# Kernel optimization log

Measured on AMD Instinct MI355X. Metric: run time of the kernel, lower is better.

Reference implementation:

```python
import jax, jax.numpy as jnp
import numpy as np


def setup_inputs() -> dict:
    key = jax.random.key(0)
    ks = jax.random.split(key, 9)
    B, H = 8192, 1024
    scale = 1.0 / np.sqrt(4 * H)
    return {
        "h": jax.random.normal(ks[0], (B, H), jnp.float32),
        "x": jax.random.normal(ks[1], (B, 2 * H), jnp.float32),
        "glo": jax.random.normal(ks[2], (B, H), jnp.float32),
        "Wi_w": jax.random.normal(ks[3], (H, 4 * H), jnp.float32) * scale,
        "Wi_b": jnp.zeros((H,), jnp.float32),
        "Wf_w": jax.random.normal(ks[4], (H, 4 * H), jnp.float32) * scale,
        "Wf_b": jnp.zeros((H,), jnp.float32),
        "Wc_w": jax.random.normal(ks[5], (H, 4 * H), jnp.float32) * scale,
        "Wc_b": jnp.zeros((H,), jnp.float32),
    }


def reference(h, x, glo, Wi_w, Wi_b, Wf_w, Wf_b, Wc_w, Wc_b):
    # Dropout is identity in eval mode (deterministic reference).
    cat_all = jnp.concatenate([h, x, glo], axis=-1)  # [B, 4H]
    # Fused gate GEMM: stack the three weight matrices, one matmul.
    W = jnp.concatenate([Wi_w, Wf_w, Wc_w], axis=0)      # [3H, 4H]
    b = jnp.concatenate([Wi_b, Wf_b, Wc_b], axis=0)      # [3H]
    gates = cat_all @ W.T + b                             # [B, 3H]
    H = h.shape[-1]
    i = jax.nn.sigmoid(gates[:, :H])
    f = jax.nn.sigmoid(gates[:, H:2 * H])
    c = jnp.tanh(gates[:, 2 * H:])
    # 2-way softmax over (i, f): alpha0 = exp(i)/(exp(i)+exp(f)) = sigmoid(i-f)
    alpha0 = jax.nn.sigmoid(i - f)
    output = alpha0 * c + (1.0 - alpha0) * h
    return output
```

## Files before the change

### kernel.cpp

```cpp
#include <hip/hip_runtime.h>

typedef unsigned short USHORT;
typedef short bf16x8 __attribute__((ext_vector_type(8)));
typedef float f32x4 __attribute__((ext_vector_type(4)));

__device__ __forceinline__ USHORT f2bf(float f) {
    unsigned u = __float_as_uint(f);
    u += 0x7fffu + ((u >> 16) & 1u);
    return (USHORT)(u >> 16);
}
__device__ __forceinline__ float bf2f(USHORT s) {
    return __uint_as_float(((unsigned)s) << 16);
}
__device__ __forceinline__ float sigm(float v) { return 1.f / (1.f + __expf(-v)); }
__device__ __forceinline__ float mytanh(float v) { return 1.f - 2.f / (__expf(2.f * v) + 1.f); }

using gcu32p = const unsigned int __attribute__((address_space(1))) *;
using lu32p  = unsigned int __attribute__((address_space(3))) *;

__device__ __forceinline__ void load_lds16(const void* g, void* l) {
    __builtin_amdgcn_global_load_lds((gcu32p)g, (lu32p)l, 16, 0, 0);
}

__global__ __launch_bounds__(256) void conv_all(const float* __restrict__ h,
                                                const float* __restrict__ x,
                                                const float* __restrict__ glo,
                                                const float* __restrict__ Wi,
                                                const float* __restrict__ Wf,
                                                const float* __restrict__ Wc,
                                                USHORT* __restrict__ A,
                                                USHORT* __restrict__ W) {
    int bid = blockIdx.x;
    if (bid < 16384) {
        int idx = (bid * 256 + threadIdx.x) * 8;
        int m = idx >> 12, k = idx & 4095;
        const float* s;
        if (k < 1024)      s = h   + (size_t)m * 1024 + k;
        else if (k < 3072) s = x   + (size_t)m * 2048 + (k - 1024);
        else               s = glo + (size_t)m * 1024 + (k - 3072);
        float4 f0 = ((const float4*)s)[0];
        float4 f1 = ((const float4*)s)[1];
        union { USHORT us[8]; uint4 v; } u;
        u.us[0] = f2bf(f0.x); u.us[1] = f2bf(f0.y); u.us[2] = f2bf(f0.z); u.us[3] = f2bf(f0.w);
        u.us[4] = f2bf(f1.x); u.us[5] = f2bf(f1.y); u.us[6] = f2bf(f1.z); u.us[7] = f2bf(f1.w);
        *(uint4*)(A + idx) = u.v;
    } else {
        int idx = ((bid - 16384) * 256 + threadIdx.x) * 8;
        int n = idx >> 12, k = idx & 4095;
        const float* base = (n < 1024) ? Wi : (n < 2048 ? Wf : Wc);
        const float* s = base + (size_t)(n & 1023) * 4096 + k;
        float4 f0 = ((const float4*)s)[0];
        float4 f1 = ((const float4*)s)[1];
        union { USHORT us[8]; uint4 v; } u;
        u.us[0] = f2bf(f0.x); u.us[1] = f2bf(f0.y); u.us[2] = f2bf(f0.z); u.us[3] = f2bf(f0.w);
        u.us[4] = f2bf(f1.x); u.us[5] = f2bf(f1.y); u.us[6] = f2bf(f1.z); u.us[7] = f2bf(f1.w);
        *(uint4*)(W + idx) = u.v;
    }
}


#define A_ELEMS 16384
#define B_ELEMS 12288

template<int ISS, int WMODE>
__device__ __forceinline__ void do_tile(const USHORT* aRd, const USHORT* bRd,
                                        USHORT* aWr, USHORT* bWr,
                                        const USHORT* (&aG)[4], const USHORT* (&bG)[3],
                                        int koff0, f32x4 (&acc)[8][3]) {
    bf16x8 bv[3][2];
    #pragma unroll
    for (int q = 0; q < 4; ++q) {
        bf16x8 av[2][2];
        #pragma unroll
        for (int m2 = 0; m2 < 2; ++m2)
            #pragma unroll
            for (int kh = 0; kh < 2; ++kh)
                av[m2][kh] = *(const bf16x8*)(aRd + (q * 32 + m2 * 16) * 64 + (koff0 ^ (kh * 32)));
        if (q == 0) {
            #pragma unroll
            for (int nt = 0; nt < 3; ++nt)
                #pragma unroll
                for (int kh = 0; kh < 2; ++kh)
                    bv[nt][kh] = *(const bf16x8*)(bRd + nt * 16 * 64 + (koff0 ^ (kh * 32)));
        }
        if (ISS) {
            if (q == 0) {
                load_lds16(aG[0], aWr);
                load_lds16(aG[1], aWr + 4096);
                aG[0] += 64; aG[1] += 64;
            } else if (q == 1) {
                load_lds16(aG[2], aWr + 8192);
                load_lds16(aG[3], aWr + 12288);
                aG[2] += 64; aG[3] += 64;
            } else if (q == 2) {
                load_lds16(bG[0], bWr);
                load_lds16(bG[1], bWr + 4096);
                bG[0] += 64; bG[1] += 64;
            } else {
                load_lds16(bG[2], bWr + 8192);
                bG[2] += 64;
            }
        }
        __builtin_amdgcn_sched_barrier(0);
        __builtin_amdgcn_s_barrier();
        __builtin_amdgcn_s_setprio(1);
        #pragma unroll
        for (int m2 = 0; m2 < 2; ++m2)
            #pragma unroll
            for (int nt = 0; nt < 3; ++nt)
                #pragma unroll
                for (int kh = 0; kh < 2; ++kh)
                    acc[q * 2 + m2][nt] = __builtin_amdgcn_mfma_f32_16x16x32_bf16(
                        av[m2][kh], bv[nt][kh], acc[q * 2 + m2][nt], 0, 0, 0);
        __builtin_amdgcn_s_setprio(0);
        if (q == 3) {
            if (WMODE == 0) asm volatile("s_waitcnt vmcnt(7)" ::: "memory");
            else if (WMODE == 1) asm volatile("s_waitcnt vmcnt(0)" ::: "memory");
        }
        __builtin_amdgcn_s_barrier();
    }
}

__global__ __launch_bounds__(512, 2) void gemm8p(const USHORT* __restrict__ A,
                                                 const USHORT* __restrict__ B,
                                                 const float* __restrict__ bi,
                                                 const float* __restrict__ bfp,
                                                 const float* __restrict__ bc,
                                                 USHORT* __restrict__ gates) {
    __shared__ __align__(16) USHORT As[3 * 256 * 64];
    __shared__ __align__(16) USHORT Bs[2 * 192 * 64];

    const int tid  = threadIdx.x;
    const int lane = tid & 63, wv = tid >> 6;
    const int s  = (blockIdx.x & 7) * 64 + (blockIdx.x >> 3);
    const int m0 = (s & 31) * 256;
    const int n0 = (s >> 5) * 192;

    const int wM = wv >> 2, wN = wv & 3;
    const int lm = lane & 15;
    const int gw = lane >> 4;
    const int koff0 = ((gw ^ (lm >> 1)) & 7) * 8;
    const int wvOff = wv * 512;
    const int aOff = (wM * 128 + lm) * 64;
    const int bOff = (wN * 48 + lm) * 64;

    const int gswz = ((lane & 7) ^ (4 * (wv & 1) + (lane >> 4))) & 7;
    const USHORT* aG[4];
    const USHORT* bG[3];
    #pragma unroll
    for (int j = 0; j < 4; ++j)
        aG[j] = A + (size_t)(m0 + j * 64 + wv * 8 + (lane >> 3)) * 4096 + gswz * 8;
    #pragma unroll
    for (int t = 0; t < 3; ++t)
        bG[t] = B + (size_t)(n0 + t * 64 + wv * 8 + (lane >> 3)) * 4096 + gswz * 8;

    f32x4 acc[8][3];
    #pragma unroll
    for (int a = 0; a < 8; ++a)
        #pragma unroll
        for (int b = 0; b < 3; ++b) {
            f32x4 z = {0.f, 0.f, 0.f, 0.f};
            acc[a][b] = z;
        }

    USHORT* aB0 = As;
    USHORT* aB1 = As + A_ELEMS;
    USHORT* aB2 = As + 2 * A_ELEMS;
    USHORT* bB0 = Bs;
    USHORT* bB1 = Bs + B_ELEMS;

    #pragma unroll
    for (int j = 0; j < 4; ++j) { load_lds16(aG[j], aB0 + j * 4096 + wvOff); aG[j] += 64; }
    #pragma unroll
    for (int t = 0; t < 3; ++t) { load_lds16(bG[t], bB0 + t * 4096 + wvOff); bG[t] += 64; }
    #pragma unroll
    for (int j = 0; j < 4; ++j) { load_lds16(aG[j], aB1 + j * 4096 + wvOff); aG[j] += 64; }
    #pragma unroll
    for (int t = 0; t < 3; ++t) { load_lds16(bG[t], bB1 + t * 4096 + wvOff); bG[t] += 64; }
    asm volatile("s_waitcnt vmcnt(7)" ::: "memory");
    __builtin_amdgcn_s_barrier();

    for (int kt = 0; kt < 62; ++kt) {
        do_tile<1, 0>(aB0 + aOff, bB0 + bOff, aB2 + wvOff, bB0 + wvOff,
                      aG, bG, koff0, acc);
        USHORT* tp = aB0; aB0 = aB1; aB1 = aB2; aB2 = tp;
        tp = bB0; bB0 = bB1; bB1 = tp;
    }
    do_tile<0, 1>(aB0 + aOff, bB0 + bOff, As, Bs, aG, bG, koff0, acc);
    do_tile<0, 2>(aB1 + aOff, bB1 + bOff, As, Bs, aG, bG, koff0, acc);

    #pragma unroll
    for (int nt = 0; nt < 3; ++nt) {
        int gc = n0 + wN * 48 + nt * 16 + lm;
        float bb = (gc < 1024) ? bi[gc] : (gc < 2048 ? bfp[gc - 1024] : bc[gc - 2048]);
        #pragma unroll
        for (int mt = 0; mt < 8; ++mt) {
            #pragma unroll
            for (int r = 0; r < 4; ++r) {
                int lrow = wM * 128 + mt * 16 + (lane >> 4) * 4 + r;
                gates[(size_t)(m0 + lrow) * 3072 + gc] = f2bf(acc[mt][nt][r] + bb);
            }
        }
    }
}

__global__ __launch_bounds__(256) void epi(const USHORT* __restrict__ gates,
                                           const float* __restrict__ h,
                                           float* __restrict__ out) {
    int e = (blockIdx.x * 256 + threadIdx.x) * 8;
    int m = e >> 10, n = e & 1023;
    const USHORT* gp = gates + (size_t)m * 3072 + n;
    union { USHORT us[8]; uint4 v; } gi, gf, gc;
    gi.v = *(const uint4*)(gp);
    gf.v = *(const uint4*)(gp + 1024);
    gc.v = *(const uint4*)(gp + 2048);
    const float* hp = h + (size_t)m * 1024 + n;
    float4 h0 = ((const float4*)hp)[0];
    float4 h1 = ((const float4*)hp)[1];
    float hv[8] = {h0.x, h0.y, h0.z, h0.w, h1.x, h1.y, h1.z, h1.w};
    float o[8];
    #pragma unroll
    for (int j = 0; j < 8; ++j) {
        float iv = sigm(bf2f(gi.us[j]));
        float fv = sigm(bf2f(gf.us[j]));
        float cv = mytanh(bf2f(gc.us[j]));
        float al = sigm(iv - fv);
        o[j] = al * cv + (1.f - al) * hv[j];
    }
    float4* op = (float4*)(out + (size_t)m * 1024 + n);
    op[0] = make_float4(o[0], o[1], o[2], o[3]);
    op[1] = make_float4(o[4], o[5], o[6], o[7]);
}

__global__ __launch_bounds__(256) void gemm3_noconv(const float* __restrict__ h,
                                                    const float* __restrict__ x,
                                                    const float* __restrict__ glo,
                                                    const float* __restrict__ Wi,
                                                    const float* __restrict__ Wf,
                                                    const float* __restrict__ Wc,
                                                    const float* __restrict__ bi,
                                                    const float* __restrict__ bfp,
                                                    const float* __restrict__ bc,
                                                    float* __restrict__ out) {
    __shared__ USHORT At[128 * 32];
    __shared__ USHORT Bt[128 * 32];
    __shared__ USHORT stash[128 * 136];

    const int tid  = threadIdx.x;
    const int lane = tid & 63, wv = tid >> 6;
    const int n0 = blockIdx.x * 128;
    const int m0 = blockIdx.y * 128;
    const int wM = wv >> 1, wN = wv & 1;
    const int lm = lane & 15, qk = (lane >> 4) * 8;
    const int rowS = tid >> 1;
    const int colS = (tid & 1) * 16;

    for (int p = 0; p < 3; ++p) {
        f32x4 acc[4][4];
        #pragma unroll
        for (int a = 0; a < 4; ++a)
            #pragma unroll
            for (int b = 0; b < 4; ++b) {
                f32x4 z = {0.f, 0.f, 0.f, 0.f};
                acc[a][b] = z;
            }
        const float* Wg = (p == 0) ? Wi : (p == 1 ? Wf : Wc);

        for (int kt = 0; kt < 128; ++kt) {
            __syncthreads();
            int k = kt * 32 + colS;
            const float* s;
            if (k < 1024)      s = h   + (size_t)(m0 + rowS) * 1024 + k;
            else if (k < 3072) s = x   + (size_t)(m0 + rowS) * 2048 + (k - 1024);
            else               s = glo + (size_t)(m0 + rowS) * 1024 + (k - 3072);
            float4 f0 = ((const float4*)s)[0], f1 = ((const float4*)s)[1];
            float4 f2 = ((const float4*)s)[2], f3 = ((const float4*)s)[3];
            union { USHORT us[8]; uint4 v; } u0, u1;
            u0.us[0]=f2bf(f0.x); u0.us[1]=f2bf(f0.y); u0.us[2]=f2bf(f0.z); u0.us[3]=f2bf(f0.w);
            u0.us[4]=f2bf(f1.x); u0.us[5]=f2bf(f1.y); u0.us[6]=f2bf(f1.z); u0.us[7]=f2bf(f1.w);
            u1.us[0]=f2bf(f2.x); u1.us[1]=f2bf(f2.y); u1.us[2]=f2bf(f2.z); u1.us[3]=f2bf(f2.w);
            u1.us[4]=f2bf(f3.x); u1.us[5]=f2bf(f3.y); u1.us[6]=f2bf(f3.z); u1.us[7]=f2bf(f3.w);
            *(uint4*)(At + rowS * 32 + colS)     = u0.v;
            *(uint4*)(At + rowS * 32 + colS + 8) = u1.v;
            const float* sw = Wg + (size_t)(n0 + rowS) * 4096 + k;
            float4 w0 = ((const float4*)sw)[0], w1 = ((const float4*)sw)[1];
            float4 w2 = ((const float4*)sw)[2], w3 = ((const float4*)sw)[3];
            union { USHORT us[8]; uint4 v; } v0, v1;
            v0.us[0]=f2bf(w0.x); v0.us[1]=f2bf(w0.y); v0.us[2]=f2bf(w0.z); v0.us[3]=f2bf(w0.w);
            v0.us[4]=f2bf(w1.x); v0.us[5]=f2bf(w1.y); v0.us[6]=f2bf(w1.z); v0.us[7]=f2bf(w1.w);
            v1.us[0]=f2bf(w2.x); v1.us[1]=f2bf(w2.y); v1.us[2]=f2bf(w2.z); v1.us[3]=f2bf(w2.w);
            v1.us[4]=f2bf(w3.x); v1.us[5]=f2bf(w3.y); v1.us[6]=f2bf(w3.z); v1.us[7]=f2bf(w3.w);
            *(uint4*)(Bt + rowS * 32 + colS)     = v0.v;
            *(uint4*)(Bt + rowS * 32 + colS + 8) = v1.v;
            __syncthreads();

            bf16x8 av[4], bv[4];
            #pragma unroll
            for (int mt = 0; mt < 4; ++mt)
                av[mt] = *(const bf16x8*)(At + (wM * 64 + mt * 16 + lm) * 32 + qk);
            #pragma unroll
            for (int nt = 0; nt < 4; ++nt)
                bv[nt] = *(const bf16x8*)(Bt + (wN * 64 + nt * 16 + lm) * 32 + qk);
            #pragma unroll
            for (int mt = 0; mt < 4; ++mt)
                #pragma unroll
                for (int nt = 0; nt < 4; ++nt)
                    acc[mt][nt] = __builtin_amdgcn_mfma_f32_16x16x32_bf16(
                        av[mt], bv[nt], acc[mt][nt], 0, 0, 0);
        }

        const float* bias = (p == 0) ? bi : (p == 1 ? bfp : bc);
        #pragma unroll
        for (int nt = 0; nt < 4; ++nt) {
            int lcol = wN * 64 + nt * 16 + lm;
            float bb = bias[n0 + lcol];
            #pragma unroll
            for (int mt = 0; mt < 4; ++mt) {
                #pragma unroll
                for (int r = 0; r < 4; ++r) {
                    int lrow = wM * 64 + mt * 16 + (lane >> 4) * 4 + r;
                    float g = acc[mt][nt][r] + bb;
                    int li = lrow * 136 + lcol;
                    if (p == 0) {
                        stash[li] = f2bf(sigm(g));
                    } else if (p == 1) {
                        float iv = bf2f(stash[li]);
                        stash[li] = f2bf(sigm(iv - sigm(g)));
                    } else {
                        float al = bf2f(stash[li]);
                        float cv = mytanh(g);
                        size_t gi = (size_t)(m0 + lrow) * 1024 + (n0 + lcol);
                        out[gi] = al * cv + (1.f - al) * h[gi];
                    }
                }
            }
        }
    }
}

extern "C" void kernel_launch(void* const* d_in, const int* in_sizes, int n_in,
                              void* d_out, int out_size, void* d_ws, size_t ws_size,
                              hipStream_t stream) {
    const float* h   = (const float*)d_in[0];
    const float* x   = (const float*)d_in[1];
    const float* glo = (const float*)d_in[2];
    const float* Wi  = (const float*)d_in[3];
    const float* bi  = (const float*)d_in[4];
    const float* Wf  = (const float*)d_in[5];
    const float* bfp = (const float*)d_in[6];
    const float* Wc  = (const float*)d_in[7];
    const float* bc  = (const float*)d_in[8];
    float* out = (float*)d_out;

    const size_t szA = (size_t)8192 * 4096 * 2;
    const size_t szW = (size_t)3072 * 4096 * 2;
    const size_t szG = (size_t)8192 * 3072 * 2;

    if (ws_size >= szA + szW + szG) {
        USHORT* Abf = (USHORT*)d_ws;
        USHORT* Wbf = (USHORT*)((char*)d_ws + szA);
        USHORT* Gbf = (USHORT*)((char*)d_ws + szA + szW);
        conv_all<<<16384 + 6144, 256, 0, stream>>>(h, x, glo, Wi, Wf, Wc, Abf, Wbf);
        gemm8p<<<512, 512, 0, stream>>>(Abf, Wbf, bi, bfp, bc, Gbf);
        epi<<<4096, 256, 0, stream>>>(Gbf, h, out);
    } else {
        gemm3_noconv<<<dim3(8, 64), 256, 0, stream>>>(
            h, x, glo, Wi, Wf, Wc, bi, bfp, bc, out);
    }
}
```

Baseline: 448.2 us.

## Fuse gate epilogue into GEMM by interleaving i/f/c weight tiles per block

Each GEMM block's 192-column N tile is remapped into three 64-column slices taken from the i, f and c gate weights at the same hidden index. Each thread therefore holds all three gate pre-activations and can apply sigmoid, tanh and the blend with h directly. This removes the bf16 gates buffer in the workspace, its write and reread, and the separate epilogue launch. In exchange, the epilogue's h loads and fp32 output stores are strided per lane rather than vectorized.

Result: faster. 423.6 us (-5.5%).

```diff
diff --git a/kernel.cpp b/kernel.cpp
--- a/kernel.cpp
+++ b/kernel.cpp
@@ -81,7 +81,7 @@
             for (int nt = 0; nt < 3; ++nt)
                 #pragma unroll
                 for (int kh = 0; kh < 2; ++kh)
-                    bv[nt][kh] = *(const bf16x8*)(bRd + nt * 16 * 64 + (koff0 ^ (kh * 32)));
+                    bv[nt][kh] = *(const bf16x8*)(bRd + nt * 4096 + (koff0 ^ (kh * 32)));
         }
         if (ISS) {
             if (q == 0) {
@@ -121,12 +121,13 @@
     }
 }
 
-__global__ __launch_bounds__(512, 2) void gemm8p(const USHORT* __restrict__ A,
-                                                 const USHORT* __restrict__ B,
-                                                 const float* __restrict__ bi,
-                                                 const float* __restrict__ bfp,
-                                                 const float* __restrict__ bc,
-                                                 USHORT* __restrict__ gates) {
+__global__ __launch_bounds__(512, 2) void gemm_fused(const USHORT* __restrict__ A,
+                                                     const USHORT* __restrict__ B,
+                                                     const float* __restrict__ bi,
+                                                     const float* __restrict__ bfp,
+                                                     const float* __restrict__ bc,
+                                                     const float* __restrict__ h,
+                                                     float* __restrict__ out) {
     __shared__ __align__(16) USHORT As[3 * 256 * 64];
     __shared__ __align__(16) USHORT Bs[2 * 192 * 64];
 
@@ -134,7 +135,7 @@
     const int lane = tid & 63, wv = tid >> 6;
     const int s  = (blockIdx.x & 7) * 64 + (blockIdx.x >> 3);
     const int m0 = (s & 31) * 256;
-    const int n0 = (s >> 5) * 192;
+    const int n0 = (s >> 5) * 64;
 
     const int wM = wv >> 2, wN = wv & 3;
     const int lm = lane & 15;
@@ -142,7 +143,7 @@
     const int koff0 = ((gw ^ (lm >> 1)) & 7) * 8;
     const int wvOff = wv * 512;
     const int aOff = (wM * 128 + lm) * 64;
-    const int bOff = (wN * 48 + lm) * 64;
+    const int bOff = (wN * 16 + lm) * 64;
 
     const int gswz = ((lane & 7) ^ (4 * (wv & 1) + (lane >> 4))) & 7;
     const USHORT* aG[4];
@@ -152,7 +153,7 @@
         aG[j] = A + (size_t)(m0 + j * 64 + wv * 8 + (lane >> 3)) * 4096 + gswz * 8;
     #pragma unroll
     for (int t = 0; t < 3; ++t)
-        bG[t] = B + (size_t)(n0 + t * 64 + wv * 8 + (lane >> 3)) * 4096 + gswz * 8;
+        bG[t] = B + (size_t)(t * 1024 + n0 + wv * 8 + (lane >> 3)) * 4096 + gswz * 8;
 
     f32x4 acc[8][3];
     #pragma unroll
@@ -189,47 +190,24 @@
     do_tile<0, 1>(aB0 + aOff, bB0 + bOff, As, Bs, aG, bG, koff0, acc);
     do_tile<0, 2>(aB1 + aOff, bB1 + bOff, As, Bs, aG, bG, koff0, acc);
 
-    #pragma unroll
-    for (int nt = 0; nt < 3; ++nt) {
-        int gc = n0 + wN * 48 + nt * 16 + lm;
-        float bb = (gc < 1024) ? bi[gc] : (gc < 2048 ? bfp[gc - 1024] : bc[gc - 2048]);
-        #pragma unroll
-        for (int mt = 0; mt < 8; ++mt) {
-            #pragma unroll
-            for (int r = 0; r < 4; ++r) {
-                int lrow = wM * 128 + mt * 16 + (lane >> 4) * 4 + r;
-                gates[(size_t)(m0 + lrow) * 3072 + gc] = f2bf(acc[mt][nt][r] + bb);
-            }
-        }
-    }
-}
-
-__global__ __launch_bounds__(256) void epi(const USHORT* __restrict__ gates,
-                                           const float* __restrict__ h,
-                                           float* __restrict__ out) {
-    int e = (blockIdx.x * 256 + threadIdx.x) * 8;
-    int m = e >> 10, n = e & 1023;
-    const USHORT* gp = gates + (size_t)m * 3072 + n;
-    union { USHORT us[8]; uint4 v; } gi, gf, gc;
-    gi.v = *(const uint4*)(gp);
-    gf.v = *(const uint4*)(gp + 1024);
-    gc.v = *(const uint4*)(gp + 2048);
-    const float* hp = h + (size_t)m * 1024 + n;
-    float4 h0 = ((const float4*)hp)[0];
-    float4 h1 = ((const float4*)hp)[1];
-    float hv[8] = {h0.x, h0.y, h0.z, h0.w, h1.x, h1.y, h1.z, h1.w};
-    float o[8];
-    #pragma unroll
-    for (int j = 0; j < 8; ++j) {
-        float iv = sigm(bf2f(gi.us[j]));
-        float fv = sigm(bf2f(gf.us[j]));
-        float cv = mytanh(bf2f(gc.us[j]));
-        float al = sigm(iv - fv);
-        o[j] = al * cv + (1.f - al) * hv[j];
-    }
-    float4* op = (float4*)(out + (size_t)m * 1024 + n);
-    op[0] = make_float4(o[0], o[1], o[2], o[3]);
-    op[1] = make_float4(o[4], o[5], o[6], o[7]);
+    const int nc = n0 + wN * 16 + lm;
+    const float bbi = bi[nc], bbf = bfp[nc], bbc = bc[nc];
+    #pragma unroll
+    for (int mt = 0; mt < 8; ++mt) {
+        #pragma unroll
+        for (int r = 0; r < 4; ++r) {
+            int lrow = wM * 128 + mt * 16 + (lane >> 4) * 4 + r;
+            size_t off = (size_t)(m0 + lrow) * 1024 + nc;
+            float gi_ = acc[mt][0][r] + bbi;
+            float gf_ = acc[mt][1][r] + bbf;
+            float gc_ = acc[mt][2][r] + bbc;
+            float iv = sigm(gi_);
+            float fv = sigm(gf_);
+            float al = sigm(iv - fv);
+            float cv = mytanh(gc_);
+            out[off] = al * cv + (1.f - al) * h[off];
+        }
+    }
 }
 
 __global__ __launch_bounds__(256) void gemm3_noconv(const float* __restrict__ h,
@@ -354,15 +332,12 @@
 
     const size_t szA = (size_t)8192 * 4096 * 2;
     const size_t szW = (size_t)3072 * 4096 * 2;
-    const size_t szG = (size_t)8192 * 3072 * 2;
-
-    if (ws_size >= szA + szW + szG) {
+
+    if (ws_size >= szA + szW) {
         USHORT* Abf = (USHORT*)d_ws;
         USHORT* Wbf = (USHORT*)((char*)d_ws + szA);
-        USHORT* Gbf = (USHORT*)((char*)d_ws + szA + szW);
         conv_all<<<16384 + 6144, 256, 0, stream>>>(h, x, glo, Wi, Wf, Wc, Abf, Wbf);
-        gemm8p<<<512, 512, 0, stream>>>(Abf, Wbf, bi, bfp, bc, Gbf);
-        epi<<<4096, 256, 0, stream>>>(Gbf, h, out);
+        gemm_fused<<<512, 512, 0, stream>>>(Abf, Wbf, bi, bfp, bc, h, out);
     } else {
         gemm3_noconv<<<dim3(8, 64), 256, 0, stream>>>(
             h, x, glo, Wi, Wf, Wc, bi, bfp, bc, out);
```
